# Performance work log

Measured on AMD Instinct MI355X. Metric: run time of the kernel, lower is better.

The kernel has to match this reference:

```python
import jax, jax.numpy as jnp
import numpy as np

N_HEAD = 8
DQK = 64
DV = 64
D_IN = 512
D_OUT = 512
D_MID = 2048
B = 4
L = 2048
EPS = 1e-5


def layernorm(x):
    mu = jnp.mean(x, axis=-1, keepdims=True)
    var = jnp.mean(jnp.square(x - mu), axis=-1, keepdims=True)
    return (x - mu) / jnp.sqrt(var + EPS)


def setup_inputs() -> dict:
    key = jax.random.key(0)
    ks = jax.random.split(key, 10)
    s = 0.02
    return {
        "query": jax.random.normal(ks[0], (B, L, D_IN), jnp.float32),
        "key": jax.random.normal(ks[1], (B, L, D_IN), jnp.float32),
        "value": jax.random.normal(ks[2], (B, L, D_IN), jnp.float32),
        "mask": jnp.zeros((B, L, L), jnp.float32),
        "WQ": jax.random.normal(ks[3], (D_IN, N_HEAD * DQK), jnp.float32) * s,
        "WK": jax.random.normal(ks[4], (D_IN, N_HEAD * DQK), jnp.float32) * s,
        "WV": jax.random.normal(ks[5], (D_IN, N_HEAD * DV), jnp.float32) * s,
        "WO": jax.random.normal(ks[6], (N_HEAD * DV, D_OUT), jnp.float32) * s,
        "W1": jax.random.normal(ks[7], (D_OUT, D_MID), jnp.float32) * s,
        "W2": jax.random.normal(ks[8], (D_MID, D_OUT), jnp.float32) * s,
    }


def reference(query, key, value, mask, WQ, WK, WV, WO, W1, W2):
    bsz = query.shape[0]
    # projections -> [b, h, l, d]
    Q = (query @ WQ).reshape(bsz, -1, N_HEAD, DQK).transpose(0, 2, 1, 3)
    K = (key @ WK).reshape(bsz, -1, N_HEAD, DQK).transpose(0, 2, 1, 3)
    V = (value @ WV).reshape(bsz, -1, N_HEAD, DV).transpose(0, 2, 1, 3)
    # scaled dot-product attention with additive mask [b, 1, lq, lk]
    scores = jnp.einsum("bhqd,bhkd->bhqk", Q, K) / jnp.sqrt(jnp.float32(DQK))
    w = jax.nn.softmax(scores + mask[:, None, :, :], axis=-1)
    out = jnp.einsum("bhqk,bhkd->bhqd", w, V)
    out = out.transpose(0, 2, 1, 3).reshape(bsz, -1, N_HEAD * DV)
    out = out @ WO
    out = layernorm(query + out)
    ff = jax.nn.relu(out @ W1) @ W2
    return layernorm(out + ff)
```

## Files before the change

kernel.cpp:

```cpp
#include <hip/hip_runtime.h>
#include <hip/hip_bf16.h>

using bf16 = __bf16;
typedef __bf16 bf16x4 __attribute__((ext_vector_type(4)));
typedef __bf16 bf16x8 __attribute__((ext_vector_type(8)));
typedef float f32x4 __attribute__((ext_vector_type(4)));

static constexpr int BATCH = 4;
static constexpr int SEQ   = 2048;
static constexpr int DIN   = 512;
static constexpr int NHEAD = 8;
static constexpr int DMID  = 2048;
static constexpr int MROWS = BATCH * SEQ;

__device__ __forceinline__ void gload16(const void* g, void* l)
{
    __builtin_amdgcn_global_load_lds(
        (const __attribute__((address_space(1))) unsigned int*)g,
        (__attribute__((address_space(3))) unsigned int*)l, 16, 0, 0);
}

__global__ __launch_bounds__(256) void tw_mask(
    const float* __restrict__ WQ, const float* __restrict__ WK,
    const float* __restrict__ WV, const float* __restrict__ WO,
    const float* __restrict__ W1, const float* __restrict__ W2,
    bf16* __restrict__ WQt, bf16* __restrict__ WKt, bf16* __restrict__ WVt,
    bf16* __restrict__ WOt, bf16* __restrict__ W1t, bf16* __restrict__ W2t,
    const uint4* __restrict__ mask, int* __restrict__ flag)
{
    const int bid = blockIdx.x;
    if (bid >= 3072) {
        const uint4* p = mask + (size_t)(bid - 3072) * 4096;
        unsigned nz = 0;
#pragma unroll
        for (int i = 0; i < 16; ++i) {
            const uint4 v = p[i * 256 + threadIdx.x];
            nz |= v.x | v.y | v.z | v.w;
        }
        if (nz) atomicOr(flag, 1);
        return;
    }
    __shared__ float tile[32][33];
    const float* in; bf16* out; int ip, op, cx, ry;
    if (bid < 1024) {
        const int w = bid >> 8, idx = bid & 255;
        in  = w == 0 ? WQ  : w == 1 ? WK  : w == 2 ? WV  : WO;
        out = w == 0 ? WQt : w == 1 ? WKt : w == 2 ? WVt : WOt;
        ip = 512; op = 512; cx = idx & 15; ry = idx >> 4;
    } else if (bid < 2048) {
        const int idx = bid - 1024;
        in = W1; out = W1t; ip = 2048; op = 512; cx = idx & 63; ry = idx >> 6;
    } else {
        const int idx = bid - 2048;
        in = W2; out = W2t; ip = 512; op = 2048; cx = idx & 15; ry = idx >> 4;
    }
    const int c0 = cx * 32, r0 = ry * 32;
    const int tx = threadIdx.x & 31, ty = threadIdx.x >> 5;
    for (int i = 0; i < 32; i += 8)
        tile[ty + i][tx] = in[(size_t)(r0 + ty + i) * ip + c0 + tx];
    __syncthreads();
    for (int i = 0; i < 32; i += 8)
        out[(size_t)(c0 + ty + i) * op + r0 + tx] = (bf16)tile[tx][ty + i];
}

template <int ACT>
__global__ __launch_bounds__(256) void gemm128(const bf16* __restrict__ A,
                                               const bf16* __restrict__ Bt,
                                               bf16* __restrict__ C,
                                               int N, int K)
{
    __shared__ bf16 sA[128 * 64];
    __shared__ bf16 sB[128 * 64];

    const int t    = threadIdx.x;
    const int lane = t & 63;
    const int wave = t >> 6;
    const int wm   = wave >> 1;
    const int wn   = wave & 1;
    const int lr   = lane & 15;
    const int lq   = lane >> 4;

    const int m0 = blockIdx.y * 128;
    const int n0 = blockIdx.x * 128;

    const int srow = lane >> 3;
    const int scol = (lane & 7) * 8;

    f32x4 acc[4][4] = {};

    for (int k0 = 0; k0 < K; k0 += 64) {
        if (k0) __syncthreads();
#pragma unroll
        for (int i = 0; i < 4; ++i) {
            const int ch = wave * 4 + i;
            const int r  = ch * 8 + srow;
            gload16(A  + (size_t)(m0 + r) * K + k0 + scol, sA + ch * 512);
            gload16(Bt + (size_t)(n0 + r) * K + k0 + scol, sB + ch * 512);
        }
        __syncthreads();

#pragma unroll
        for (int kk = 0; kk < 2; ++kk) {
            bf16x8 af[4], bfr[4];
#pragma unroll
            for (int x = 0; x < 4; ++x) {
                af[x]  = *reinterpret_cast<const bf16x8*>(&sA[(wm * 64 + x * 16 + lr) * 64 + kk * 32 + lq * 8]);
                bfr[x] = *reinterpret_cast<const bf16x8*>(&sB[(wn * 64 + x * 16 + lr) * 64 + kk * 32 + lq * 8]);
            }
#pragma unroll
            for (int m = 0; m < 4; ++m)
#pragma unroll
                for (int n = 0; n < 4; ++n)
                    acc[m][n] = __builtin_amdgcn_mfma_f32_16x16x32_bf16(af[m], bfr[n], acc[m][n], 0, 0, 0);
        }
    }

#pragma unroll
    for (int n = 0; n < 4; ++n) {
        const int col = n0 + wn * 64 + n * 16 + lr;
#pragma unroll
        for (int m = 0; m < 4; ++m) {
            const int rowb = m0 + wm * 64 + m * 16 + lq * 4;
#pragma unroll
            for (int j = 0; j < 4; ++j) {
                float v = acc[m][n][j];
                if (ACT == 1) v = v > 0.f ? v : 0.f;
                C[(size_t)(rowb + j) * N + col] = (bf16)v;
            }
        }
    }
}

__global__ __launch_bounds__(256) void gemm64_qkv(const float* __restrict__ q,
                                                  const float* __restrict__ k,
                                                  const float* __restrict__ v,
                                                  const bf16* __restrict__ WQt,
                                                  const bf16* __restrict__ WKt,
                                                  const bf16* __restrict__ WVt,
                                                  bf16* __restrict__ Qb,
                                                  bf16* __restrict__ Kb,
                                                  bf16* __restrict__ Vt)
{
    __shared__ bf16 sA[64 * 64];
    __shared__ bf16 sB[128 * 64];

    const float* A  = blockIdx.z == 0 ? q   : blockIdx.z == 1 ? k   : v;
    const bf16*  Bt = blockIdx.z == 0 ? WQt : blockIdx.z == 1 ? WKt : WVt;
    const int K = DIN;

    const int t    = threadIdx.x;
    const int lane = t & 63;
    const int wave = t >> 6;
    const int lr   = lane & 15;
    const int lq   = lane >> 4;

    const int m0 = blockIdx.y * 64;
    const int n0 = blockIdx.x * 128;

    const int srow = lane >> 3;
    const int scol = (lane & 7) * 8;

    f32x4 acc[4][2] = {};

    for (int k0 = 0; k0 < K; k0 += 64) {
        float4 fa[4];
#pragma unroll
        for (int i = 0; i < 2; ++i) {
            const float* p = A + (size_t)(m0 + (wave * 2 + i) * 8 + srow) * K + k0 + scol;
            fa[2 * i]     = *reinterpret_cast<const float4*>(p);
            fa[2 * i + 1] = *reinterpret_cast<const float4*>(p + 4);
        }
        if (k0) __syncthreads();
#pragma unroll
        for (int i = 0; i < 4; ++i) {
            const int ch = wave * 4 + i;
            gload16(Bt + (size_t)(n0 + ch * 8 + srow) * K + k0 + scol, sB + ch * 512);
        }
#pragma unroll
        for (int i = 0; i < 2; ++i) {
            const int r = (wave * 2 + i) * 8 + srow;
            const float4 a = fa[2 * i], b = fa[2 * i + 1];
            bf16x8 hh;
            hh[0] = (bf16)a.x; hh[1] = (bf16)a.y; hh[2] = (bf16)a.z; hh[3] = (bf16)a.w;
            hh[4] = (bf16)b.x; hh[5] = (bf16)b.y; hh[6] = (bf16)b.z; hh[7] = (bf16)b.w;
            *reinterpret_cast<bf16x8*>(&sA[r * 64 + scol]) = hh;
        }
        __syncthreads();

#pragma unroll
        for (int kk = 0; kk < 2; ++kk) {
            bf16x8 af[4], bfr[2];
#pragma unroll
            for (int x = 0; x < 4; ++x)
                af[x] = *reinterpret_cast<const bf16x8*>(&sA[(x * 16 + lr) * 64 + kk * 32 + lq * 8]);
#pragma unroll
            for (int n = 0; n < 2; ++n)
                bfr[n] = *reinterpret_cast<const bf16x8*>(&sB[(wave * 32 + n * 16 + lr) * 64 + kk * 32 + lq * 8]);
#pragma unroll
            for (int m = 0; m < 4; ++m)
#pragma unroll
                for (int n = 0; n < 2; ++n)
                    acc[m][n] = __builtin_amdgcn_mfma_f32_16x16x32_bf16(af[m], bfr[n], acc[m][n], 0, 0, 0);
        }
    }

    if (blockIdx.z < 2) {
        bf16* C = blockIdx.z == 0 ? Qb : Kb;
#pragma unroll
        for (int n = 0; n < 2; ++n) {
            const int col = n0 + wave * 32 + n * 16 + lr;
#pragma unroll
            for (int m = 0; m < 4; ++m) {
                const int rowb = m0 + m * 16 + lq * 4;
#pragma unroll
                for (int j = 0; j < 4; ++j)
                    C[(size_t)(rowb + j) * DIN + col] = (bf16)acc[m][n][j];
            }
        }
    } else {
        __syncthreads();
#pragma unroll
        for (int n = 0; n < 2; ++n)
#pragma unroll
            for (int m = 0; m < 4; ++m)
#pragma unroll
                for (int j = 0; j < 4; ++j)
                    sB[(wave * 32 + n * 16 + lr) * 64 + m * 16 + lq * 4 + j] = (bf16)acc[m][n][j];
        __syncthreads();
        const int c = t >> 1, half = t & 1;
#pragma unroll
        for (int qq = 0; qq < 4; ++qq) {
            const bf16x8 vv = *reinterpret_cast<const bf16x8*>(&sB[c * 64 + half * 32 + qq * 8]);
            *reinterpret_cast<bf16x8*>(Vt + (size_t)(n0 + c) * MROWS + m0 + half * 32 + qq * 8) = vv;
        }
    }
}

__global__ __launch_bounds__(256) void attn_kernel(const bf16* __restrict__ Qb,
                                                   const bf16* __restrict__ Kb,
                                                   const bf16* __restrict__ Vt,
                                                   const float* __restrict__ mask,
                                                   bf16* __restrict__ O,
                                                   const int* __restrict__ mzf)
{
    const int bi   = blockIdx.x;
    const int xcd  = bi & 7;
    const int slot = bi >> 3;
    const int pair = xcd * 4 + (slot >> 4);
    const int qt   = slot & 15;
    const int h    = pair >> 2;
    const int b    = pair & 3;

    const int t    = threadIdx.x;
    const int lane = t & 63;
    const int wave = t >> 6;
    const int lr   = lane & 15;
    const int lq   = lane >> 4;
    const int q0   = qt * 128;
    const bool useM = (*mzf != 0);

    __shared__ bf16 sK[64 * 72];
    __shared__ bf16 sV[64 * 72];
    __shared__ bf16 sP[4][32 * 72];
    __shared__ bf16 sM[128 * 68];

    bf16x8 qf[2][2];
#pragma unroll
    for (int g = 0; g < 2; ++g) {
        const int qrow = q0 + wave * 32 + g * 16 + lr;
        const bf16* qp = Qb + (size_t)(b * SEQ + qrow) * DIN + h * 64 + lq * 8;
        qf[g][0] = *reinterpret_cast<const bf16x8*>(qp);
        qf[g][1] = *reinterpret_cast<const bf16x8*>(qp + 32);
    }

    f32x4 o[2][4] = {};
    f32x4 lrow[2] = {};

    const int sr = t >> 2;
    const int sc = (t & 3) << 3;

    const bf16*  kbase = Kb + (size_t)(b * SEQ) * DIN + h * 64;
    const bf16*  vbase = Vt + (size_t)(h * 64 + sr) * MROWS + b * SEQ;
    const float* mbase = mask + ((size_t)b * SEQ + q0) * SEQ;

    constexpr float L2E = 1.4426950408889634f;
    constexpr float SCL = 0.125f * L2E;
    const bf16x8 ones = {(bf16)1.f, (bf16)1.f, (bf16)1.f, (bf16)1.f,
                         (bf16)1.f, (bf16)1.f, (bf16)1.f, (bf16)1.f};

    int4 kr0 = *reinterpret_cast<const int4*>(kbase + (size_t)sr * DIN + sc);
    int4 kr1 = *reinterpret_cast<const int4*>(kbase + (size_t)sr * DIN + sc + 32);
    int4 vr0 = *reinterpret_cast<const int4*>(vbase + sc);
    int4 vr1 = *reinterpret_cast<const int4*>(vbase + sc + 32);

    for (int tile = 0; tile < SEQ / 64; ++tile) {
        if (tile) __syncthreads();

        *reinterpret_cast<int4*>(&sK[sr * 72 + sc])      = kr0;
        *reinterpret_cast<int4*>(&sK[sr * 72 + sc + 32]) = kr1;
        *reinterpret_cast<int4*>(&sV[sr * 72 + sc])      = vr0;
        *reinterpret_cast<int4*>(&sV[sr * 72 + sc + 32]) = vr1;
        if (useM) {
            const int k0 = tile * 64;
#pragma unroll
            for (int i = 0; i < 8; ++i) {
                const int idx = t + 256 * i;
                const float4 mr = *reinterpret_cast<const float4*>(
                    mbase + (size_t)(idx >> 4) * SEQ + k0 + (idx & 15) * 4);
                bf16x4 mv;
                mv[0] = (bf16)(mr.x * L2E); mv[1] = (bf16)(mr.y * L2E);
                mv[2] = (bf16)(mr.z * L2E); mv[3] = (bf16)(mr.w * L2E);
                *reinterpret_cast<bf16x4*>(&sM[(idx >> 4) * 68 + (idx & 15) * 4]) = mv;
            }
        }

        if (tile + 1 < SEQ / 64) {
            const int k0 = (tile + 1) * 64;
            kr0 = *reinterpret_cast<const int4*>(kbase + (size_t)(k0 + sr) * DIN + sc);
            kr1 = *reinterpret_cast<const int4*>(kbase + (size_t)(k0 + sr) * DIN + sc + 32);
            vr0 = *reinterpret_cast<const int4*>(vbase + k0 + sc);
            vr1 = *reinterpret_cast<const int4*>(vbase + k0 + sc + 32);
        }
        __syncthreads();

        bf16x8 kf[2][4];
#pragma unroll
        for (int s = 0; s < 2; ++s)
#pragma unroll
            for (int ni = 0; ni < 4; ++ni)
                kf[s][ni] = *reinterpret_cast<const bf16x8*>(&sK[(ni * 16 + lr) * 72 + s * 32 + lq * 8]);

#pragma unroll
        for (int g = 0; g < 2; ++g) {
            f32x4 sf[4] = {};
#pragma unroll
            for (int s = 0; s < 2; ++s)
#pragma unroll
                for (int ni = 0; ni < 4; ++ni)
                    sf[ni] = __builtin_amdgcn_mfma_f32_16x16x32_bf16(qf[g][s], kf[s][ni], sf[ni], 0, 0, 0);

            if (useM) {
#pragma unroll
                for (int j = 0; j < 4; ++j) {
                    const int mr2 = (wave * 32 + g * 16 + lq * 4 + j) * 68;
#pragma unroll
                    for (int ni = 0; ni < 4; ++ni) {
                        const float mval = (float)sM[mr2 + ni * 16 + lr];
                        sP[wave][(g * 16 + lq * 4 + j) * 72 + ni * 16 + lr] = (bf16)exp2f(sf[ni][j] * SCL + mval);
                    }
                }
            } else {
#pragma unroll
                for (int j = 0; j < 4; ++j)
#pragma unroll
                    for (int ni = 0; ni < 4; ++ni)
                        sP[wave][(g * 16 + lq * 4 + j) * 72 + ni * 16 + lr] = (bf16)exp2f(sf[ni][j] * SCL);
            }
        }

        bf16x8 vf[2][4];
#pragma unroll
        for (int s = 0; s < 2; ++s)
#pragma unroll
            for (int ni = 0; ni < 4; ++ni)
                vf[s][ni] = *reinterpret_cast<const bf16x8*>(&sV[(ni * 16 + lr) * 72 + s * 32 + lq * 8]);

#pragma unroll
        for (int g = 0; g < 2; ++g) {
            f32x4 rs = {};
#pragma unroll
            for (int s = 0; s < 2; ++s) {
                bf16x8 pf = *reinterpret_cast<const bf16x8*>(&sP[wave][(g * 16 + lr) * 72 + s * 32 + lq * 8]);
                rs = __builtin_amdgcn_mfma_f32_16x16x32_bf16(pf, ones, rs, 0, 0, 0);
#pragma unroll
                for (int ni = 0; ni < 4; ++ni)
                    o[g][ni] = __builtin_amdgcn_mfma_f32_16x16x32_bf16(pf, vf[s][ni], o[g][ni], 0, 0, 0);
            }
#pragma unroll
            for (int j = 0; j < 4; ++j)
                lrow[g][j] += rs[j];
        }
    }

#pragma unroll
    for (int g = 0; g < 2; ++g)
#pragma unroll
        for (int ni = 0; ni < 4; ++ni)
#pragma unroll
            for (int j = 0; j < 4; ++j) {
                const int row = q0 + wave * 32 + g * 16 + lq * 4 + j;
                const int col = h * 64 + ni * 16 + lr;
                O[(size_t)(b * SEQ + row) * DIN + col] = (bf16)(o[g][ni][j] / lrow[g][j]);
            }
}

__global__ __launch_bounds__(512) void gemm_ln(const bf16* __restrict__ A,
                                               const bf16* __restrict__ Bt,
                                               const float* __restrict__ X,
                                               bf16* __restrict__ Onb,
                                               float* __restrict__ Onf,
                                               int K)
{
    __shared__ bf16 sA[2][32 * 64];
    __shared__ bf16 sB[2][512 * 64];
    __shared__ float sRed[32][8];
    __shared__ float sMu[32];
    __shared__ float sRstd[32];

    const int t    = threadIdx.x;
    const int lane = t & 63;
    const int w    = t >> 6;
    const int lr   = lane & 15;
    const int lq   = lane >> 4;
    const int srow = lane >> 3;
    const int scol = (lane & 7) * 8;

    const int m0 = blockIdx.x * 32;

    auto stage = [&](int s, int b) {
        const int k0 = s * 64;
#pragma unroll
        for (int i = 0; i < 8; ++i) {
            const int ch = w * 8 + i;
            gload16(Bt + (size_t)(ch * 8 + srow) * K + k0 + scol, &sB[b][ch * 512]);
        }
        if (w < 4)
            gload16(A + (size_t)(m0 + w * 8 + srow) * K + k0 + scol, &sA[b][w * 512]);
    };

    f32x4 acc[2][4] = {};
    const int steps = K / 64;

    stage(0, 0);
    __syncthreads();

    for (int s = 0; s < steps; ++s) {
        const int b = s & 1;
        if (s + 1 < steps) stage(s + 1, b ^ 1);

#pragma unroll
        for (int kk = 0; kk < 2; ++kk) {
            bf16x8 af[2], bfr[4];
#pragma unroll
            for (int m = 0; m < 2; ++m)
                af[m] = *reinterpret_cast<const bf16x8*>(&sA[b][(m * 16 + lr) * 64 + kk * 32 + lq * 8]);
#pragma unroll
            for (int n = 0; n < 4; ++n)
                bfr[n] = *reinterpret_cast<const bf16x8*>(&sB[b][(w * 64 + n * 16 + lr) * 64 + kk * 32 + lq * 8]);
#pragma unroll
            for (int m = 0; m < 2; ++m)
#pragma unroll
                for (int n = 0; n < 4; ++n)
                    acc[m][n] = __builtin_amdgcn_mfma_f32_16x16x32_bf16(af[m], bfr[n], acc[m][n], 0, 0, 0);
        }
        __syncthreads();
    }

#pragma unroll
    for (int m = 0; m < 2; ++m)
#pragma unroll
        for (int n = 0; n < 4; ++n)
#pragma unroll
            for (int j = 0; j < 4; ++j)
                acc[m][n][j] += X[(size_t)(m0 + m * 16 + lq * 4 + j) * DIN + w * 64 + n * 16 + lr];

#pragma unroll
    for (int m = 0; m < 2; ++m)
#pragma unroll
        for (int j = 0; j < 4; ++j) {
            float s = acc[m][0][j] + acc[m][1][j] + acc[m][2][j] + acc[m][3][j];
            s += __shfl_xor(s, 1); s += __shfl_xor(s, 2);
            s += __shfl_xor(s, 4); s += __shfl_xor(s, 8);
            if (lr == 0) sRed[m * 16 + lq * 4 + j][w] = s;
        }
    __syncthreads();
    if (t < 32) {
        float s = 0.f;
#pragma unroll
        for (int ww = 0; ww < 8; ++ww) s += sRed[t][ww];
        sMu[t] = s * (1.f / DIN);
    }
    __syncthreads();

#pragma unroll
    for (int m = 0; m < 2; ++m)
#pragma unroll
        for (int j = 0; j < 4; ++j) {
            const float mu = sMu[m * 16 + lq * 4 + j];
            float s = 0.f;
#pragma unroll
            for (int n = 0; n < 4; ++n) {
                const float d = acc[m][n][j] - mu;
                s += d * d;
            }
            s += __shfl_xor(s, 1); s += __shfl_xor(s, 2);
            s += __shfl_xor(s, 4); s += __shfl_xor(s, 8);
            if (lr == 0) sRed[m * 16 + lq * 4 + j][w] = s;
        }
    __syncthreads();
    if (t < 32) {
        float s = 0.f;
#pragma unroll
        for (int ww = 0; ww < 8; ++ww) s += sRed[t][ww];
        sRstd[t] = rsqrtf(s * (1.f / DIN) + 1e-5f);
    }
    __syncthreads();

#pragma unroll
    for (int m = 0; m < 2; ++m)
#pragma unroll
        for (int j = 0; j < 4; ++j) {
            const int rl = m * 16 + lq * 4 + j;
            const float mu = sMu[rl], rstd = sRstd[rl];
            const size_t rowoff = (size_t)(m0 + rl) * DIN;
#pragma unroll
            for (int n = 0; n < 4; ++n) {
                const float r = (acc[m][n][j] - mu) * rstd;
                const int col = w * 64 + n * 16 + lr;
                if (Onb) Onb[rowoff + col] = (bf16)r;
                if (Onf) Onf[rowoff + col] = r;
            }
        }
}

extern "C" void kernel_launch(void* const* d_in, const int* in_sizes, int n_in,
                              void* d_out, int out_size, void* d_ws, size_t ws_size,
                              hipStream_t stream)
{
    const float* query = (const float*)d_in[0];
    const float* key   = (const float*)d_in[1];
    const float* value = (const float*)d_in[2];
    const float* mask  = (const float*)d_in[3];
    const float* WQ    = (const float*)d_in[4];
    const float* WK    = (const float*)d_in[5];
    const float* WV    = (const float*)d_in[6];
    const float* WO    = (const float*)d_in[7];
    const float* W1    = (const float*)d_in[8];
    const float* W2    = (const float*)d_in[9];

    char* w = (char*)d_ws;
    size_t off = 0;
    auto carve2 = [&](size_t elems) { bf16* p = (bf16*)(w + off); off += elems * 2; return p; };
    auto carve4 = [&](size_t elems) { float* p = (float*)(w + off); off += elems * 4; return p; };

    bf16* Qb    = carve2((size_t)MROWS * DIN);
    bf16* Kb    = carve2((size_t)MROWS * DIN);
    bf16* Vb    = carve2((size_t)MROWS * DIN);
    bf16* Vt    = carve2((size_t)MROWS * DIN);
    bf16* Mid   = carve2((size_t)MROWS * DMID);
    float* Ln1f = carve4((size_t)MROWS * DIN);
    bf16* WQt   = carve2((size_t)DIN * DIN);
    bf16* WKt   = carve2((size_t)DIN * DIN);
    bf16* WVt   = carve2((size_t)DIN * DIN);
    bf16* WOt   = carve2((size_t)DIN * DIN);
    bf16* W1t   = carve2((size_t)DIN * DMID);
    bf16* W2t   = carve2((size_t)DMID * DIN);
    int*  mzf   = (int*)(w + off); off += 16;
    if (off > ws_size) return;

    bf16* Ob   = Vb;
    bf16* Ln1b = Kb;

    const dim3 blk(256);

    hipMemsetAsync(mzf, 0, 4, stream);

    tw_mask<<<dim3(4096), blk, 0, stream>>>(WQ, WK, WV, WO, W1, W2,
                                            WQt, WKt, WVt, WOt, W1t, W2t,
                                            (const uint4*)mask, mzf);

    gemm64_qkv<<<dim3(DIN / 128, MROWS / 64, 3), blk, 0, stream>>>(query, key, value,
                                                                   WQt, WKt, WVt, Qb, Kb, Vt);

    attn_kernel<<<dim3(512), blk, 0, stream>>>(Qb, Kb, Vt, mask, Ob, mzf);

    gemm_ln<<<dim3(MROWS / 32), dim3(512), 0, stream>>>(Ob, WOt, query, Ln1b, Ln1f, DIN);

    gemm128<1><<<dim3(DMID / 128, MROWS / 128), blk, 0, stream>>>(Ln1b, W1t, Mid, DMID, DIN);

    gemm_ln<<<dim3(MROWS / 32), dim3(512), 0, stream>>>(Mid, W2t, Ln1f,
                                                        (bf16*)nullptr, (float*)d_out, DMID);
}
```

Before: 370.4 us.

## Pre-convert QKV inputs to bf16 and use LDS transpose reads for P in attention

The prep kernel now also converts the fp32 query/key/value activations to bf16 in a separate buffer (reusing the Mid scratch space). The QKV projection GEMM can then stage A tiles through direct global-to-LDS loads instead of loading fp32 into registers and converting. Separately, the attention kernel writes P transposed into LDS and reads it back with ds_read_b64_tr_b16, and raises wave priority around the MFMA blocks. The aim is less register staging in the GEMM and cheaper P fragment loads, at the cost of an extra pass over the inputs and explicit waitcnt and scheduling barriers.

After: 376.3 us. Within noise of the previous version (+1.6%).

```diff
diff --git a/kernel.cpp b/kernel.cpp
--- a/kernel.cpp
+++ b/kernel.cpp
@@ -20,22 +20,47 @@
         (__attribute__((address_space(3))) unsigned int*)l, 16, 0, 0);
 }
 
+__device__ __forceinline__ bf16x4 ds_tr16(const bf16* p)
+{
+    bf16x4 r;
+    auto lp = (const __attribute__((address_space(3))) bf16*)p;
+    asm volatile("ds_read_b64_tr_b16 %0, %1" : "=&v"(r) : "v"(lp) : "memory");
+    return r;
+}
+
 __global__ __launch_bounds__(256) void tw_mask(
     const float* __restrict__ WQ, const float* __restrict__ WK,
     const float* __restrict__ WV, const float* __restrict__ WO,
     const float* __restrict__ W1, const float* __restrict__ W2,
     bf16* __restrict__ WQt, bf16* __restrict__ WKt, bf16* __restrict__ WVt,
     bf16* __restrict__ WOt, bf16* __restrict__ W1t, bf16* __restrict__ W2t,
+    const float* __restrict__ q, const float* __restrict__ k,
+    const float* __restrict__ v,
+    bf16* __restrict__ qb, bf16* __restrict__ kb, bf16* __restrict__ vb,
     const uint4* __restrict__ mask, int* __restrict__ flag)
 {
     const int bid = blockIdx.x;
+    if (bid >= 4096) {
+        const int idx = bid - 4096;
+        const float* src = idx < 1024 ? q : idx < 2048 ? k : v;
+        bf16*       dst = idx < 1024 ? qb : idx < 2048 ? kb : vb;
+        const size_t b4 = (size_t)(idx & 1023) * 1024;
+#pragma unroll
+        for (int i = 0; i < 4; ++i) {
+            const float4 f = reinterpret_cast<const float4*>(src)[b4 + i * 256 + threadIdx.x];
+            bf16x4 h;
+            h[0] = (bf16)f.x; h[1] = (bf16)f.y; h[2] = (bf16)f.z; h[3] = (bf16)f.w;
+            reinterpret_cast<bf16x4*>(dst)[b4 + i * 256 + threadIdx.x] = h;
+        }
+        return;
+    }
     if (bid >= 3072) {
         const uint4* p = mask + (size_t)(bid - 3072) * 4096;
         unsigned nz = 0;
 #pragma unroll
         for (int i = 0; i < 16; ++i) {
-            const uint4 v = p[i * 256 + threadIdx.x];
-            nz |= v.x | v.y | v.z | v.w;
+            const uint4 u = p[i * 256 + threadIdx.x];
+            nz |= u.x | u.y | u.z | u.w;
         }
         if (nz) atomicOr(flag, 1);
         return;
@@ -131,21 +156,21 @@
     }
 }
 
-__global__ __launch_bounds__(256) void gemm64_qkv(const float* __restrict__ q,
-                                                  const float* __restrict__ k,
-                                                  const float* __restrict__ v,
-                                                  const bf16* __restrict__ WQt,
-                                                  const bf16* __restrict__ WKt,
-                                                  const bf16* __restrict__ WVt,
-                                                  bf16* __restrict__ Qb,
-                                                  bf16* __restrict__ Kb,
-                                                  bf16* __restrict__ Vt)
+__global__ __launch_bounds__(256) void gemm64_qkvb(const bf16* __restrict__ qb,
+                                                   const bf16* __restrict__ kb,
+                                                   const bf16* __restrict__ vb,
+                                                   const bf16* __restrict__ WQt,
+                                                   const bf16* __restrict__ WKt,
+                                                   const bf16* __restrict__ WVt,
+                                                   bf16* __restrict__ Qb,
+                                                   bf16* __restrict__ Kb,
+                                                   bf16* __restrict__ Vt)
 {
     __shared__ bf16 sA[64 * 64];
     __shared__ bf16 sB[128 * 64];
 
-    const float* A  = blockIdx.z == 0 ? q   : blockIdx.z == 1 ? k   : v;
-    const bf16*  Bt = blockIdx.z == 0 ? WQt : blockIdx.z == 1 ? WKt : WVt;
+    const bf16* A  = blockIdx.z == 0 ? qb  : blockIdx.z == 1 ? kb  : vb;
+    const bf16* Bt = blockIdx.z == 0 ? WQt : blockIdx.z == 1 ? WKt : WVt;
     const int K = DIN;
 
     const int t    = threadIdx.x;
@@ -163,27 +188,16 @@
     f32x4 acc[4][2] = {};
 
     for (int k0 = 0; k0 < K; k0 += 64) {
-        float4 fa[4];
+        if (k0) __syncthreads();
 #pragma unroll
         for (int i = 0; i < 2; ++i) {
-            const float* p = A + (size_t)(m0 + (wave * 2 + i) * 8 + srow) * K + k0 + scol;
-            fa[2 * i]     = *reinterpret_cast<const float4*>(p);
-            fa[2 * i + 1] = *reinterpret_cast<const float4*>(p + 4);
-        }
-        if (k0) __syncthreads();
+            const int ch = wave * 2 + i;
+            gload16(A + (size_t)(m0 + ch * 8 + srow) * K + k0 + scol, sA + ch * 512);
+        }
 #pragma unroll
         for (int i = 0; i < 4; ++i) {
             const int ch = wave * 4 + i;
             gload16(Bt + (size_t)(n0 + ch * 8 + srow) * K + k0 + scol, sB + ch * 512);
-        }
-#pragma unroll
-        for (int i = 0; i < 2; ++i) {
-            const int r = (wave * 2 + i) * 8 + srow;
-            const float4 a = fa[2 * i], b = fa[2 * i + 1];
-            bf16x8 hh;
-            hh[0] = (bf16)a.x; hh[1] = (bf16)a.y; hh[2] = (bf16)a.z; hh[3] = (bf16)a.w;
-            hh[4] = (bf16)b.x; hh[5] = (bf16)b.y; hh[6] = (bf16)b.z; hh[7] = (bf16)b.w;
-            *reinterpret_cast<bf16x8*>(&sA[r * 64 + scol]) = hh;
         }
         __syncthreads();
 
@@ -261,7 +275,7 @@
 
     __shared__ bf16 sK[64 * 72];
     __shared__ bf16 sV[64 * 72];
-    __shared__ bf16 sP[4][32 * 72];
+    __shared__ bf16 sPT[4][2048];
     __shared__ bf16 sM[128 * 68];
 
     bf16x8 qf[2][2];
@@ -333,49 +347,65 @@
 #pragma unroll
         for (int g = 0; g < 2; ++g) {
             f32x4 sf[4] = {};
+            __builtin_amdgcn_s_setprio(1);
 #pragma unroll
             for (int s = 0; s < 2; ++s)
 #pragma unroll
                 for (int ni = 0; ni < 4; ++ni)
                     sf[ni] = __builtin_amdgcn_mfma_f32_16x16x32_bf16(qf[g][s], kf[s][ni], sf[ni], 0, 0, 0);
-
-            if (useM) {
-#pragma unroll
-                for (int j = 0; j < 4; ++j) {
-                    const int mr2 = (wave * 32 + g * 16 + lq * 4 + j) * 68;
-#pragma unroll
-                    for (int ni = 0; ni < 4; ++ni) {
-                        const float mval = (float)sM[mr2 + ni * 16 + lr];
-                        sP[wave][(g * 16 + lq * 4 + j) * 72 + ni * 16 + lr] = (bf16)exp2f(sf[ni][j] * SCL + mval);
+            __builtin_amdgcn_s_setprio(0);
+
+#pragma unroll
+            for (int ni = 0; ni < 4; ++ni) {
+                bf16x4 pw;
+                if (useM) {
+#pragma unroll
+                    for (int j = 0; j < 4; ++j) {
+                        const float mval = (float)sM[(wave * 32 + g * 16 + lq * 4 + j) * 68 + ni * 16 + lr];
+                        pw[j] = (bf16)exp2f(sf[ni][j] * SCL + mval);
                     }
+                } else {
+#pragma unroll
+                    for (int j = 0; j < 4; ++j)
+                        pw[j] = (bf16)exp2f(sf[ni][j] * SCL);
                 }
-            } else {
-#pragma unroll
-                for (int j = 0; j < 4; ++j)
-#pragma unroll
-                    for (int ni = 0; ni < 4; ++ni)
-                        sP[wave][(g * 16 + lq * 4 + j) * 72 + ni * 16 + lr] = (bf16)exp2f(sf[ni][j] * SCL);
-            }
-        }
-
-        bf16x8 vf[2][4];
+                *reinterpret_cast<bf16x4*>(&sPT[wave][g * 1024 + (ni * 16 + lr) * 16 + lq * 4]) = pw;
+            }
+        }
+
+        bf16x8 vfr[2][4];
 #pragma unroll
         for (int s = 0; s < 2; ++s)
 #pragma unroll
             for (int ni = 0; ni < 4; ++ni)
-                vf[s][ni] = *reinterpret_cast<const bf16x8*>(&sV[(ni * 16 + lr) * 72 + s * 32 + lq * 8]);
+                vfr[s][ni] = *reinterpret_cast<const bf16x8*>(&sV[(ni * 16 + lr) * 72 + s * 32 + lq * 8]);
+
+        asm volatile("s_waitcnt lgkmcnt(0)" ::: "memory");
+        __builtin_amdgcn_sched_barrier(0);
 
 #pragma unroll
         for (int g = 0; g < 2; ++g) {
+            const bf16* pb = &sPT[wave][g * 1024 + lq * 128 + lr];
+            const bf16x4 t00 = ds_tr16(pb);
+            const bf16x4 t01 = ds_tr16(pb + 64);
+            const bf16x4 t10 = ds_tr16(pb + 512);
+            const bf16x4 t11 = ds_tr16(pb + 576);
+            asm volatile("s_waitcnt lgkmcnt(0)" ::: "memory");
+            __builtin_amdgcn_sched_barrier(0);
+            const bf16x8 pa0 = __builtin_shufflevector(t00, t01, 0, 1, 2, 3, 4, 5, 6, 7);
+            const bf16x8 pa1 = __builtin_shufflevector(t10, t11, 0, 1, 2, 3, 4, 5, 6, 7);
+
+            __builtin_amdgcn_s_setprio(1);
             f32x4 rs = {};
-#pragma unroll
-            for (int s = 0; s < 2; ++s) {
-                bf16x8 pf = *reinterpret_cast<const bf16x8*>(&sP[wave][(g * 16 + lr) * 72 + s * 32 + lq * 8]);
-                rs = __builtin_amdgcn_mfma_f32_16x16x32_bf16(pf, ones, rs, 0, 0, 0);
-#pragma unroll
-                for (int ni = 0; ni < 4; ++ni)
-                    o[g][ni] = __builtin_amdgcn_mfma_f32_16x16x32_bf16(pf, vf[s][ni], o[g][ni], 0, 0, 0);
-            }
+            rs = __builtin_amdgcn_mfma_f32_16x16x32_bf16(pa0, ones, rs, 0, 0, 0);
+#pragma unroll
+            for (int ni = 0; ni < 4; ++ni)
+                o[g][ni] = __builtin_amdgcn_mfma_f32_16x16x32_bf16(pa0, vfr[0][ni], o[g][ni], 0, 0, 0);
+            rs = __builtin_amdgcn_mfma_f32_16x16x32_bf16(pa1, ones, rs, 0, 0, 0);
+#pragma unroll
+            for (int ni = 0; ni < 4; ++ni)
+                o[g][ni] = __builtin_amdgcn_mfma_f32_16x16x32_bf16(pa1, vfr[1][ni], o[g][ni], 0, 0, 0);
+            __builtin_amdgcn_s_setprio(0);
 #pragma unroll
             for (int j = 0; j < 4; ++j)
                 lrow[g][j] += rs[j];
@@ -560,17 +590,21 @@
 
     bf16* Ob   = Vb;
     bf16* Ln1b = Kb;
+    bf16* qb = Mid;
+    bf16* kb = Mid + (size_t)MROWS * DIN;
+    bf16* vb = Mid + (size_t)2 * MROWS * DIN;
 
     const dim3 blk(256);
 
     hipMemsetAsync(mzf, 0, 4, stream);
 
-    tw_mask<<<dim3(4096), blk, 0, stream>>>(WQ, WK, WV, WO, W1, W2,
+    tw_mask<<<dim3(7168), blk, 0, stream>>>(WQ, WK, WV, WO, W1, W2,
                                             WQt, WKt, WVt, WOt, W1t, W2t,
+                                            query, key, value, qb, kb, vb,
                                             (const uint4*)mask, mzf);
 
-    gemm64_qkv<<<dim3(DIN / 128, MROWS / 64, 3), blk, 0, stream>>>(query, key, value,
-                                                                   WQt, WKt, WVt, Qb, Kb, Vt);
+    gemm64_qkvb<<<dim3(DIN / 128, MROWS / 64, 3), blk, 0, stream>>>(qb, kb, vb,
+                                                                    WQt, WKt, WVt, Qb, Kb, Vt);
 
     attn_kernel<<<dim3(512), blk, 0, stream>>>(Qb, Kb, Vt, mask, Ob, mzf);
 
```
